# Kernel optimization log

Hardware: AMD Instinct MI355X
Metric: run time of the kernel (lower is better)

The kernel has to match this reference:

```python
import jax, jax.numpy as jnp
import numpy as np

THR = 1.0  # snntorch Leaky default threshold


def _heaviside(u):
    return (u > 0).astype(u.dtype)


def setup_inputs() -> dict:
    key = jax.random.key(0)
    ks = jax.random.split(key, 5)
    B, n_inp, n_hid = 4096, 1024, 256
    x = jax.random.normal(ks[0], (B, n_inp), dtype=jnp.float32)
    # PyTorch Linear init scale ~ 1/sqrt(fan_in)
    W1 = jax.random.normal(ks[1], (n_hid, n_inp), dtype=jnp.float32) / np.sqrt(n_inp)
    b1 = jax.random.normal(ks[2], (n_hid,), dtype=jnp.float32) / np.sqrt(n_inp)
    W2 = jax.random.normal(ks[3], (1, n_hid), dtype=jnp.float32) / np.sqrt(n_hid)
    b2 = jax.random.normal(ks[4], (1,), dtype=jnp.float32) / np.sqrt(n_hid)
    return {"x": x, "W1": W1, "b1": b1, "W2": W2, "b2": b2}


def reference(x, W1, b1, W2, b2):
    beta = jnp.float32(0.9)  # leaky
    T = x.shape[1]  # forward loops range(x.size(1)) with the SAME input
    # fc1(x) is loop-invariant in the original; compute once (same math).
    cur1 = x @ W1.T + b1  # [B, n_hid]
    B, n_hid = cur1.shape

    def step(carry, _):
        mem1, mem2 = carry
        # snntorch Leaky: reset from PREVIOUS mem (detached), subtract mechanism
        reset1 = _heaviside(mem1 - THR)
        mem1 = beta * mem1 + cur1 - reset1 * THR
        spk1 = _heaviside(mem1 - THR)
        cur2 = spk1 @ W2.T + b2  # [B, 1]
        reset2 = _heaviside(mem2 - THR)
        mem2 = beta * mem2 + cur2 - reset2 * THR
        spk2 = _heaviside(mem2 - THR)
        return (mem1, mem2), (mem2, spk2)

    init = (jnp.zeros((B, n_hid), x.dtype), jnp.zeros((B, 1), x.dtype))
    _, (mem2_rec, spk2_rec) = jax.lax.scan(step, init, None, length=T)
    # [T, B, 1] each, matching the list-of-steps in the torch code
    return mem2_rec, spk2_rec
```

## Files before the change

### kernel.cpp

```cpp
#include <hip/hip_runtime.h>
#include <stdint.h>


#define GEMM_TILE 64
#define GEMM_KC 16

__global__ __launch_bounds__(256) void fc1_gemm_panel(
    const float* __restrict__ x, const float* __restrict__ W1,
    float* __restrict__ p1, float* __restrict__ p2) {
  constexpr int K = 1024, N = 256, KP = 512;
  __shared__ float As[GEMM_KC][GEMM_TILE + 4];
  __shared__ float Ws[GEMM_KC][GEMM_TILE + 4];

  const int tid = threadIdx.x;
  const int b0 = blockIdx.x * GEMM_TILE;
  const int h0 = blockIdx.y * GEMM_TILE;
  const int kbase = blockIdx.z * KP;
  float* __restrict__ outp = blockIdx.z ? p2 : p1;

  const int tx = tid & 15;
  const int ty = tid >> 4;
  const int srow = tid >> 2;
  const int scol = (tid & 3) << 2;

  const float* xp = x + (size_t)(b0 + srow) * K + kbase + scol;
  const float* wp = W1 + (size_t)(h0 + srow) * K + kbase + scol;

  float4 av = *reinterpret_cast<const float4*>(xp);
  float4 wv = *reinterpret_cast<const float4*>(wp);

  float acc[4][4] = {};

  for (int kc = 0; kc < KP; kc += GEMM_KC) {
    __syncthreads();
    As[scol + 0][srow] = av.x; As[scol + 1][srow] = av.y;
    As[scol + 2][srow] = av.z; As[scol + 3][srow] = av.w;
    Ws[scol + 0][srow] = wv.x; Ws[scol + 1][srow] = wv.y;
    Ws[scol + 2][srow] = wv.z; Ws[scol + 3][srow] = wv.w;
    __syncthreads();
    if (kc + GEMM_KC < KP) {
      av = *reinterpret_cast<const float4*>(xp + kc + GEMM_KC);
      wv = *reinterpret_cast<const float4*>(wp + kc + GEMM_KC);
    }
#pragma unroll
    for (int kk = 0; kk < GEMM_KC; ++kk) {
      float4 a4 = *reinterpret_cast<const float4*>(&As[kk][ty << 2]);
      float4 w4 = *reinterpret_cast<const float4*>(&Ws[kk][tx << 2]);
      float af[4] = {a4.x, a4.y, a4.z, a4.w};
      float wf[4] = {w4.x, w4.y, w4.z, w4.w};
#pragma unroll
      for (int i = 0; i < 4; ++i)
#pragma unroll
        for (int j = 0; j < 4; ++j)
          acc[i][j] = fmaf(af[i], wf[j], acc[i][j]);
    }
  }

#pragma unroll
  for (int i = 0; i < 4; ++i) {
    float4 o = make_float4(acc[i][0], acc[i][1], acc[i][2], acc[i][3]);
    *reinterpret_cast<float4*>(
        &outp[(size_t)(b0 + (ty << 2) + i) * N + h0 + (tx << 2)]) = o;
  }
}

__global__ __launch_bounds__(256) void snn_phase1(
    const float* __restrict__ p1, const float* __restrict__ p2,
    const float* __restrict__ b1, float* __restrict__ mem1buf,
    unsigned long long* __restrict__ sbuf, int t0, int tc) {
  __shared__ unsigned long long lds[4][64];
  const int b = blockIdx.x;
  const int h = threadIdx.x;
  const int lane = h & 63;
  const int w = h >> 6;
  const float c =
      __fadd_rn(__fadd_rn(p1[b * 256 + h], p2[b * 256 + h]), b1[h]);
  float m = (t0 == 0) ? 0.0f : mem1buf[b * 256 + h];
  float sp = (m > 1.0f) ? 1.0f : 0.0f;

  unsigned long long* __restrict__ wbase = sbuf + (size_t)(b * 4 + w) * tc;

  for (int tb = 0; tb < tc; tb += 64) {
#pragma unroll
    for (int u = 0; u < 64; ++u) {
      m = __fsub_rn(__fadd_rn(__fmul_rn(m, 0.9f), c), sp);
      const bool s = m > 1.0f;
      const unsigned long long bal = __ballot(s);
      sp = s ? 1.0f : 0.0f;
      if (lane == 0) lds[w][u] = bal;
    }
    wbase[tb + lane] = lds[w][lane];
  }
  mem1buf[b * 256 + h] = m;
}

__global__ __launch_bounds__(256) void snn_phase2(
    const unsigned long long* __restrict__ sbuf, const float* __restrict__ W2,
    float* __restrict__ cur2ws, int t0, int tc, int tcshift) {
  const int id = blockIdx.x * 256 + threadIdx.x;
  const int b = id >> tcshift;
  const int tl = id & (tc - 1);

  uint32_t wd[8];
#pragma unroll
  for (int w = 0; w < 4; ++w) {
    const unsigned long long v = sbuf[(size_t)(b * 4 + w) * tc + tl];
    wd[2 * w] = (uint32_t)v;
    wd[2 * w + 1] = (uint32_t)(v >> 32);
  }
  const int* w2i = reinterpret_cast<const int*>(W2);

  float p[8] = {0.f, 0.f, 0.f, 0.f, 0.f, 0.f, 0.f, 0.f};
#pragma unroll
  for (int j = 0; j < 32; ++j) {
#pragma unroll
    for (int l = 0; l < 8; ++l) {
      const int h = 8 * j + l;
      const int mask = -(int)((wd[h >> 5] >> (h & 31)) & 1u);
      p[l] = __fadd_rn(p[l], __int_as_float(mask & w2i[h]));
    }
  }
  const float q0 = __fadd_rn(p[0], p[4]);
  const float q1 = __fadd_rn(p[1], p[5]);
  const float q2 = __fadd_rn(p[2], p[6]);
  const float q3 = __fadd_rn(p[3], p[7]);
  const float acc = __fadd_rn(__fadd_rn(q0, q2), __fadd_rn(q1, q3));

  cur2ws[(size_t)b * 1024 + (t0 + tl)] = acc;
}

__global__ __launch_bounds__(64) void snn_phase3(
    const float* __restrict__ cur2ws, const float* __restrict__ b2,
    float* __restrict__ out) {
  const int b = blockIdx.x * 64 + threadIdx.x;
  const float b2s = b2[0];
  float m2 = 0.0f, sp2 = 0.0f;
  float* __restrict__ outm = out;
  float* __restrict__ outs = out + (size_t)1024 * 4096;
  const float4* __restrict__ s4 =
      reinterpret_cast<const float4*>(cur2ws + (size_t)b * 1024);

  float4 b0 = s4[0], b1v = s4[1], b2v = s4[2], b3 = s4[3];

#define SCAN4(V, TBASE)                                               \
  {                                                                   \
    const float vals[4] = {V.x, V.y, V.z, V.w};                       \
    _Pragma("unroll") for (int u = 0; u < 4; ++u) {                   \
      const size_t idx = (size_t)((TBASE) + u) * 4096 + b;            \
      const float cur2 = __fadd_rn(vals[u], b2s);                     \
      m2 = __fsub_rn(__fadd_rn(__fmul_rn(m2, 0.9f), cur2), sp2);      \
      const bool s = m2 > 1.0f;                                       \
      outm[idx] = m2;                                                 \
      const float sf = s ? 1.0f : 0.0f;                               \
      outs[idx] = sf;                                                 \
      sp2 = sf;                                                       \
    }                                                                 \
  }

  for (int g = 0; g < 63; ++g) {
    const float4 c0 = b0, c1 = b1v, c2 = b2v, c3 = b3;
    const int nb = (g + 1) * 4;
    b0 = s4[nb + 0]; b1v = s4[nb + 1]; b2v = s4[nb + 2]; b3 = s4[nb + 3];
    const int tb = g * 16;
    SCAN4(c0, tb); SCAN4(c1, tb + 4); SCAN4(c2, tb + 8); SCAN4(c3, tb + 12);
  }
  SCAN4(b0, 1008); SCAN4(b1v, 1012); SCAN4(b2v, 1016); SCAN4(b3, 1020);
#undef SCAN4
}

extern "C" void kernel_launch(void* const* d_in, const int* in_sizes, int n_in,
                              void* d_out, int out_size, void* d_ws,
                              size_t ws_size, hipStream_t stream) {
  const float* x = (const float*)d_in[0];
  const float* W1 = (const float*)d_in[1];
  const float* b1 = (const float*)d_in[2];
  const float* W2 = (const float*)d_in[3];
  const float* b2 = (const float*)d_in[4];
  float* out = (float*)d_out;

  constexpr int T = 1024, B = 4096;
  float* p1buf = (float*)d_ws;
  float* p2buf = (float*)((char*)d_ws + (4u << 20));
  float* mem1buf = (float*)((char*)d_ws + (8u << 20));
  float* cur2ws = (float*)((char*)d_ws + (12u << 20));
  unsigned long long* sbuf =
      (unsigned long long*)((char*)d_ws + (28u << 20));

  size_t avail = (ws_size > (size_t)(28u << 20)) ? ws_size - (28u << 20) : 0;
  int Tc = 64, shift = 6;
  while (Tc < T && (size_t)(Tc * 2) * (B * 32) <= avail) { Tc <<= 1; ++shift; }

  dim3 gemm_grid(B / GEMM_TILE, 256 / GEMM_TILE, 2);
  fc1_gemm_panel<<<gemm_grid, 256, 0, stream>>>(x, W1, p1buf, p2buf);

  for (int t0 = 0; t0 < T; t0 += Tc) {
    const int tc = (T - t0 < Tc) ? (T - t0) : Tc;
    snn_phase1<<<B, 256, 0, stream>>>(p1buf, p2buf, b1, mem1buf, sbuf, t0, tc);
    snn_phase2<<<(B / 256) * tc, 256, 0, stream>>>(sbuf, W2, cur2ws, t0, tc,
                                                   shift);
  }
  snn_phase3<<<B / 64, 64, 0, stream>>>(cur2ws, b2, out);
}
```

Baseline: 314.5 us.

## Double-buffer GEMM shared tiles and give each SNN thread two neurons

The fc1 GEMM now keeps two shared-memory buffers, so the next K-chunk is written into the spare buffer while the current one is consumed. This cuts the two barriers per iteration down to one. The phase1 recurrence now has each thread carry two independent neuron chains, with two batch rows per block. That halves the block count and interleaves two dependent FMA/ballot sequences to hide latency, at the cost of more registers and a larger LDS footprint.

```diff
diff --git a/kernel.cpp b/kernel.cpp
--- a/kernel.cpp
+++ b/kernel.cpp
@@ -9,8 +9,8 @@
     const float* __restrict__ x, const float* __restrict__ W1,
     float* __restrict__ p1, float* __restrict__ p2) {
   constexpr int K = 1024, N = 256, KP = 512;
-  __shared__ float As[GEMM_KC][GEMM_TILE + 4];
-  __shared__ float Ws[GEMM_KC][GEMM_TILE + 4];
+  __shared__ float As[2][GEMM_KC][GEMM_TILE + 4];
+  __shared__ float Ws[2][GEMM_KC][GEMM_TILE + 4];
 
   const int tid = threadIdx.x;
   const int b0 = blockIdx.x * GEMM_TILE;
@@ -28,24 +28,25 @@
 
   float4 av = *reinterpret_cast<const float4*>(xp);
   float4 wv = *reinterpret_cast<const float4*>(wp);
+  As[0][scol + 0][srow] = av.x; As[0][scol + 1][srow] = av.y;
+  As[0][scol + 2][srow] = av.z; As[0][scol + 3][srow] = av.w;
+  Ws[0][scol + 0][srow] = wv.x; Ws[0][scol + 1][srow] = wv.y;
+  Ws[0][scol + 2][srow] = wv.z; Ws[0][scol + 3][srow] = wv.w;
+  __syncthreads();
 
   float acc[4][4] = {};
+  int cur = 0;
 
   for (int kc = 0; kc < KP; kc += GEMM_KC) {
-    __syncthreads();
-    As[scol + 0][srow] = av.x; As[scol + 1][srow] = av.y;
-    As[scol + 2][srow] = av.z; As[scol + 3][srow] = av.w;
-    Ws[scol + 0][srow] = wv.x; Ws[scol + 1][srow] = wv.y;
-    Ws[scol + 2][srow] = wv.z; Ws[scol + 3][srow] = wv.w;
-    __syncthreads();
-    if (kc + GEMM_KC < KP) {
+    const bool more = (kc + GEMM_KC < KP);
+    if (more) {
       av = *reinterpret_cast<const float4*>(xp + kc + GEMM_KC);
       wv = *reinterpret_cast<const float4*>(wp + kc + GEMM_KC);
     }
 #pragma unroll
     for (int kk = 0; kk < GEMM_KC; ++kk) {
-      float4 a4 = *reinterpret_cast<const float4*>(&As[kk][ty << 2]);
-      float4 w4 = *reinterpret_cast<const float4*>(&Ws[kk][tx << 2]);
+      float4 a4 = *reinterpret_cast<const float4*>(&As[cur][kk][ty << 2]);
+      float4 w4 = *reinterpret_cast<const float4*>(&Ws[cur][kk][tx << 2]);
       float af[4] = {a4.x, a4.y, a4.z, a4.w};
       float wf[4] = {w4.x, w4.y, w4.z, w4.w};
 #pragma unroll
@@ -53,6 +54,15 @@
 #pragma unroll
         for (int j = 0; j < 4; ++j)
           acc[i][j] = fmaf(af[i], wf[j], acc[i][j]);
+    }
+    if (more) {
+      const int nxt = cur ^ 1;
+      As[nxt][scol + 0][srow] = av.x; As[nxt][scol + 1][srow] = av.y;
+      As[nxt][scol + 2][srow] = av.z; As[nxt][scol + 3][srow] = av.w;
+      Ws[nxt][scol + 0][srow] = wv.x; Ws[nxt][scol + 1][srow] = wv.y;
+      Ws[nxt][scol + 2][srow] = wv.z; Ws[nxt][scol + 3][srow] = wv.w;
+      __syncthreads();
+      cur = nxt;
     }
   }
 
@@ -68,30 +78,48 @@
     const float* __restrict__ p1, const float* __restrict__ p2,
     const float* __restrict__ b1, float* __restrict__ mem1buf,
     unsigned long long* __restrict__ sbuf, int t0, int tc) {
-  __shared__ unsigned long long lds[4][64];
-  const int b = blockIdx.x;
-  const int h = threadIdx.x;
-  const int lane = h & 63;
-  const int w = h >> 6;
-  const float c =
-      __fadd_rn(__fadd_rn(p1[b * 256 + h], p2[b * 256 + h]), b1[h]);
-  float m = (t0 == 0) ? 0.0f : mem1buf[b * 256 + h];
-  float sp = (m > 1.0f) ? 1.0f : 0.0f;
-
-  unsigned long long* __restrict__ wbase = sbuf + (size_t)(b * 4 + w) * tc;
+  __shared__ unsigned long long lds[2][4][64];
+  const int tid = threadIdx.x;
+  const int lane = tid & 63;
+  const int w = (tid >> 6) & 1;
+  const int r = tid >> 7;
+  const int b = (blockIdx.x << 1) + r;
+  const int hlo = (w << 6) + lane;
+  const int hhi = hlo + 128;
+
+  const float cA =
+      __fadd_rn(__fadd_rn(p1[b * 256 + hlo], p2[b * 256 + hlo]), b1[hlo]);
+  const float cB =
+      __fadd_rn(__fadd_rn(p1[b * 256 + hhi], p2[b * 256 + hhi]), b1[hhi]);
+  float mA = (t0 == 0) ? 0.0f : mem1buf[b * 256 + hlo];
+  float mB = (t0 == 0) ? 0.0f : mem1buf[b * 256 + hhi];
+  float spA = (mA > 1.0f) ? 1.0f : 0.0f;
+  float spB = (mB > 1.0f) ? 1.0f : 0.0f;
+
+  unsigned long long* __restrict__ wbA = sbuf + (size_t)(b * 4 + w) * tc;
+  unsigned long long* __restrict__ wbB = sbuf + (size_t)(b * 4 + w + 2) * tc;
 
   for (int tb = 0; tb < tc; tb += 64) {
 #pragma unroll
     for (int u = 0; u < 64; ++u) {
-      m = __fsub_rn(__fadd_rn(__fmul_rn(m, 0.9f), c), sp);
-      const bool s = m > 1.0f;
-      const unsigned long long bal = __ballot(s);
-      sp = s ? 1.0f : 0.0f;
-      if (lane == 0) lds[w][u] = bal;
-    }
-    wbase[tb + lane] = lds[w][lane];
-  }
-  mem1buf[b * 256 + h] = m;
+      mA = __fsub_rn(__fadd_rn(__fmul_rn(mA, 0.9f), cA), spA);
+      mB = __fsub_rn(__fadd_rn(__fmul_rn(mB, 0.9f), cB), spB);
+      const bool sA = mA > 1.0f;
+      const bool sB = mB > 1.0f;
+      const unsigned long long balA = __ballot(sA);
+      const unsigned long long balB = __ballot(sB);
+      spA = sA ? 1.0f : 0.0f;
+      spB = sB ? 1.0f : 0.0f;
+      if (lane == 0) {
+        lds[r][w][u] = balA;
+        lds[r][w + 2][u] = balB;
+      }
+    }
+    wbA[tb + lane] = lds[r][w][lane];
+    wbB[tb + lane] = lds[r][w + 2][lane];
+  }
+  mem1buf[b * 256 + hlo] = mA;
+  mem1buf[b * 256 + hhi] = mB;
 }
 
 __global__ __launch_bounds__(256) void snn_phase2(
@@ -195,7 +223,8 @@
 
   for (int t0 = 0; t0 < T; t0 += Tc) {
     const int tc = (T - t0 < Tc) ? (T - t0) : Tc;
-    snn_phase1<<<B, 256, 0, stream>>>(p1buf, p2buf, b1, mem1buf, sbuf, t0, tc);
+    snn_phase1<<<B / 2, 256, 0, stream>>>(p1buf, p2buf, b1, mem1buf, sbuf, t0,
+                                          tc);
     snn_phase2<<<(B / 256) * tc, 256, 0, stream>>>(sbuf, W2, cur2ws, t0, tc,
                                                    shift);
   }
```

New measurement: 325.7 us. 3.6% more time.

## Double-buffer GEMM shared tiles and replace per-step ballots with a bit-matrix transpose

Applied to the files above, without the earlier changes.

The fc1 GEMM now uses double-buffered LDS tiles, so the next chunk is written while the current one is consumed, needing one barrier per iteration instead of two. In phase1, each lane packs its own 64 spike bits into registers, and a shuffle-based 64x64 bit transpose produces the per-timestep ballot words. This replaces the 64 ballots and LDS writes per chunk. The cost is extra shuffle and bitwise ALU work per chunk.

```diff
diff --git a/kernel.cpp b/kernel.cpp
--- a/kernel.cpp
+++ b/kernel.cpp
@@ -9,8 +9,8 @@
     const float* __restrict__ x, const float* __restrict__ W1,
     float* __restrict__ p1, float* __restrict__ p2) {
   constexpr int K = 1024, N = 256, KP = 512;
-  __shared__ float As[GEMM_KC][GEMM_TILE + 4];
-  __shared__ float Ws[GEMM_KC][GEMM_TILE + 4];
+  __shared__ float As[2][GEMM_KC][GEMM_TILE + 4];
+  __shared__ float Ws[2][GEMM_KC][GEMM_TILE + 4];
 
   const int tid = threadIdx.x;
   const int b0 = blockIdx.x * GEMM_TILE;
@@ -28,24 +28,25 @@
 
   float4 av = *reinterpret_cast<const float4*>(xp);
   float4 wv = *reinterpret_cast<const float4*>(wp);
+  As[0][scol + 0][srow] = av.x; As[0][scol + 1][srow] = av.y;
+  As[0][scol + 2][srow] = av.z; As[0][scol + 3][srow] = av.w;
+  Ws[0][scol + 0][srow] = wv.x; Ws[0][scol + 1][srow] = wv.y;
+  Ws[0][scol + 2][srow] = wv.z; Ws[0][scol + 3][srow] = wv.w;
+  __syncthreads();
 
   float acc[4][4] = {};
+  int cur = 0;
 
   for (int kc = 0; kc < KP; kc += GEMM_KC) {
-    __syncthreads();
-    As[scol + 0][srow] = av.x; As[scol + 1][srow] = av.y;
-    As[scol + 2][srow] = av.z; As[scol + 3][srow] = av.w;
-    Ws[scol + 0][srow] = wv.x; Ws[scol + 1][srow] = wv.y;
-    Ws[scol + 2][srow] = wv.z; Ws[scol + 3][srow] = wv.w;
-    __syncthreads();
-    if (kc + GEMM_KC < KP) {
+    const bool more = (kc + GEMM_KC < KP);
+    if (more) {
       av = *reinterpret_cast<const float4*>(xp + kc + GEMM_KC);
       wv = *reinterpret_cast<const float4*>(wp + kc + GEMM_KC);
     }
 #pragma unroll
     for (int kk = 0; kk < GEMM_KC; ++kk) {
-      float4 a4 = *reinterpret_cast<const float4*>(&As[kk][ty << 2]);
-      float4 w4 = *reinterpret_cast<const float4*>(&Ws[kk][tx << 2]);
+      float4 a4 = *reinterpret_cast<const float4*>(&As[cur][kk][ty << 2]);
+      float4 w4 = *reinterpret_cast<const float4*>(&Ws[cur][kk][tx << 2]);
       float af[4] = {a4.x, a4.y, a4.z, a4.w};
       float wf[4] = {w4.x, w4.y, w4.z, w4.w};
 #pragma unroll
@@ -53,6 +54,15 @@
 #pragma unroll
         for (int j = 0; j < 4; ++j)
           acc[i][j] = fmaf(af[i], wf[j], acc[i][j]);
+    }
+    if (more) {
+      const int nxt = cur ^ 1;
+      As[nxt][scol + 0][srow] = av.x; As[nxt][scol + 1][srow] = av.y;
+      As[nxt][scol + 2][srow] = av.z; As[nxt][scol + 3][srow] = av.w;
+      Ws[nxt][scol + 0][srow] = wv.x; Ws[nxt][scol + 1][srow] = wv.y;
+      Ws[nxt][scol + 2][srow] = wv.z; Ws[nxt][scol + 3][srow] = wv.w;
+      __syncthreads();
+      cur = nxt;
     }
   }
 
@@ -64,11 +74,18 @@
   }
 }
 
+__device__ __forceinline__ uint32_t xstage(uint32_t v, int S, uint32_t M,
+                                           bool even) {
+  const uint32_t y = (uint32_t)__shfl_xor((int)v, S, 64);
+  const uint32_t a = (v & ~M) | ((y << S) & M);
+  const uint32_t b = (v & M) | ((y & M) >> S);
+  return even ? a : b;
+}
+
 __global__ __launch_bounds__(256) void snn_phase1(
     const float* __restrict__ p1, const float* __restrict__ p2,
     const float* __restrict__ b1, float* __restrict__ mem1buf,
     unsigned long long* __restrict__ sbuf, int t0, int tc) {
-  __shared__ unsigned long long lds[4][64];
   const int b = blockIdx.x;
   const int h = threadIdx.x;
   const int lane = h & 63;
@@ -80,16 +97,48 @@
 
   unsigned long long* __restrict__ wbase = sbuf + (size_t)(b * 4 + w) * tc;
 
+  const bool e32 = (lane < 32);
+  const bool e16 = ((lane & 16) == 0);
+  const bool e8 = ((lane & 8) == 0);
+  const bool e4 = ((lane & 4) == 0);
+  const bool e2 = ((lane & 2) == 0);
+  const bool e1 = ((lane & 1) == 0);
+
   for (int tb = 0; tb < tc; tb += 64) {
-#pragma unroll
-    for (int u = 0; u < 64; ++u) {
+    uint32_t lo = 0u, hi = 0u;
+#pragma unroll
+    for (int u = 0; u < 32; ++u) {
       m = __fsub_rn(__fadd_rn(__fmul_rn(m, 0.9f), c), sp);
       const bool s = m > 1.0f;
-      const unsigned long long bal = __ballot(s);
       sp = s ? 1.0f : 0.0f;
-      if (lane == 0) lds[w][u] = bal;
-    }
-    wbase[tb + lane] = lds[w][lane];
+      const uint32_t t = lo | (1u << u);
+      lo = s ? t : lo;
+    }
+#pragma unroll
+    for (int u = 0; u < 32; ++u) {
+      m = __fsub_rn(__fadd_rn(__fmul_rn(m, 0.9f), c), sp);
+      const bool s = m > 1.0f;
+      sp = s ? 1.0f : 0.0f;
+      const uint32_t t = hi | (1u << u);
+      hi = s ? t : hi;
+    }
+
+    {
+      const uint32_t ylo = (uint32_t)__shfl_xor((int)lo, 32, 64);
+      const uint32_t yhi = (uint32_t)__shfl_xor((int)hi, 32, 64);
+      const uint32_t nlo = e32 ? lo : yhi;
+      const uint32_t nhi = e32 ? ylo : hi;
+      lo = nlo;
+      hi = nhi;
+    }
+    lo = xstage(lo, 16, 0xFFFF0000u, e16); hi = xstage(hi, 16, 0xFFFF0000u, e16);
+    lo = xstage(lo, 8, 0xFF00FF00u, e8);   hi = xstage(hi, 8, 0xFF00FF00u, e8);
+    lo = xstage(lo, 4, 0xF0F0F0F0u, e4);   hi = xstage(hi, 4, 0xF0F0F0F0u, e4);
+    lo = xstage(lo, 2, 0xCCCCCCCCu, e2);   hi = xstage(hi, 2, 0xCCCCCCCCu, e2);
+    lo = xstage(lo, 1, 0xAAAAAAAAu, e1);   hi = xstage(hi, 1, 0xAAAAAAAAu, e1);
+
+    wbase[tb + lane] =
+        ((unsigned long long)hi << 32) | (unsigned long long)lo;
   }
   mem1buf[b * 256 + h] = m;
 }
```

Measured after the change: 252.5 us. -19.7%, faster.
